# Performance work log

Measured on AMD Instinct MI355X. Metric: run time of the kernel, lower is better.

The kernel has to match this reference:

```python
import jax, jax.numpy as jnp
import numpy as np
from jax import lax

OBS_LEN = 20
N_COORD = 2
HIDDEN = 192  # z_dim + s_dim = 128 + 64
N = 131072


def setup_inputs() -> dict:
    key = jax.random.key(0)
    ks = jax.random.split(key, 6)
    obs_traj_rel = jax.random.normal(ks[0], (OBS_LEN, N, N_COORD), dtype=jnp.float32)
    pred_lstm_hidden = jax.random.normal(ks[1], (N, HIDDEN), dtype=jnp.float32)
    # LSTMCell params (torch layout: weight_ih [4H, in], weight_hh [4H, H])
    w_ih = jax.random.normal(ks[2], (4 * HIDDEN, N_COORD), dtype=jnp.float32) * 0.1
    w_hh = jax.random.normal(ks[3], (4 * HIDDEN, HIDDEN), dtype=jnp.float32) * 0.1
    b_ih = jnp.zeros((4 * HIDDEN,), dtype=jnp.float32)
    b_hh = jnp.zeros((4 * HIDDEN,), dtype=jnp.float32)
    # hidden2pos Linear
    w_out = jax.random.normal(ks[4], (N_COORD, HIDDEN), dtype=jnp.float32) * 0.1
    b_out = jnp.zeros((N_COORD,), dtype=jnp.float32)
    return {
        "obs_traj_rel": obs_traj_rel,
        "pred_lstm_hidden": pred_lstm_hidden,
        "w_ih": w_ih,
        "w_hh": w_hh,
        "b_ih": b_ih,
        "b_hh": b_hh,
        "w_out": w_out,
        "b_out": b_out,
    }


def reference(obs_traj_rel, pred_lstm_hidden, w_ih, w_hh, b_ih, b_hh, w_out, b_out):
    T = obs_traj_rel.shape[0]
    # step i uses obs_traj_rel[max(i-1, 0)] -> indices [0, 0, 1, ..., T-2]
    idx = jnp.concatenate([jnp.zeros((1,), jnp.int32), jnp.arange(T - 1, dtype=jnp.int32)])
    xs = obs_traj_rel[idx, :, :N_COORD]  # [T, N, 2]

    def step(carry, x_t):
        h, c = carry
        gates = x_t @ w_ih.T + b_ih + h @ w_hh.T + b_hh  # [N, 4H]
        i, f, g, o = jnp.split(gates, 4, axis=-1)  # torch LSTMCell gate order
        i = jax.nn.sigmoid(i)
        f = jax.nn.sigmoid(f)
        g = jnp.tanh(g)
        o = jax.nn.sigmoid(o)
        c_new = f * c + i * g
        h_new = o * jnp.tanh(c_new)
        out = h_new @ w_out.T + b_out  # [N, 2]
        return (h_new, c_new), out

    c0 = jnp.zeros_like(pred_lstm_hidden)
    (_, _), outs = lax.scan(step, (pred_lstm_hidden, c0), xs)
    return outs  # [T, N, 2]
```

## Files before the change

### kernel.cpp

```cpp
#include <hip/hip_runtime.h>

typedef _Float16 half8 __attribute__((ext_vector_type(8)));
typedef float floatx4 __attribute__((ext_vector_type(4)));

#define T_STEPS 20
#define NSEQ 131072
#define HID 192
#define ROWS 32
#define HPAD 200
#define HROWS 17
#define WOFF 147456
#define XOFF 150528
#define FR_TOTAL (XOFF + 6144)

#define MFMA16(a, b, c) __builtin_amdgcn_mfma_f32_16x16x32_f16((a), (b), (c), 0, 0, 0)

__global__ void build_frags(const float* __restrict__ whh,
                            const float* __restrict__ wout,
                            const float* __restrict__ wih,
                            const float* __restrict__ bih,
                            const float* __restrict__ bhh,
                            _Float16* __restrict__ dst) {
    int i = blockIdx.x * 256 + threadIdx.x;
    if (i < WOFF) {
        int e = i & 7, L = (i >> 3) & 63, g = (i >> 9) & 3, u = i >> 11;
        int kc = u % 6, ht = u / 6;
        int n = L & 15, q = L >> 4;
        dst[i] = (_Float16)whh[(size_t)(g * HID + ht * 16 + n) * HID + kc * 32 + q * 8 + e];
    } else if (i < XOFF) {
        int k = i - WOFF;
        int e = k & 7, L = (k >> 3) & 63, kc = k >> 9;
        int n = L & 15, q = L >> 4;
        dst[i] = (_Float16)((n < 2) ? wout[n * HID + kc * 32 + q * 8 + e] : 0.f);
    } else if (i < FR_TOTAL) {
        int k = i - XOFF;
        int e = k & 7, n = (k >> 3) & 15, g = (k >> 7) & 3, ht = k >> 9;
        int col = g * HID + ht * 16 + n;
        float v = 0.f;
        if (e == 0)      v = wih[col * 2];
        else if (e == 1) v = wih[col * 2 + 1];
        else if (e == 2) v = bih[col] + bhh[col];
        dst[i] = (_Float16)v;
    }
}

__global__ __launch_bounds__(768) __attribute__((amdgpu_waves_per_eu(3, 3)))
void lstm_fused_kernel(
    const float* __restrict__ obs,
    const float* __restrict__ h0,
    const float* __restrict__ b_out,
    const _Float16* __restrict__ frags,
    float* __restrict__ out)
{
    __shared__ _Float16 h0b[2][HROWS][HPAD];
    __shared__ _Float16 h1b[HROWS][HPAD];
    __shared__ _Float16 b_lds[49152];
    __shared__ _Float16 wo_lds[3072];
    __shared__ float2 x_all[T_STEPS][ROWS];

    const int tid  = threadIdx.x;
    const int wave = tid >> 6;
    const int lane = tid & 63;
    const int quad = lane >> 4;
    const int l16  = lane & 15;
    const int ht   = wave;
    const int base = blockIdx.x * ROWS;
    const int j    = ht * 16 + l16;

    const half8 HZ = {0, 0, 0, 0, 0, 0, 0, 0};

    half8 bw[16], bx[4];
#pragma unroll
    for (int kc = 0; kc < 4; ++kc)
#pragma unroll
        for (int g = 0; g < 4; ++g)
            bw[kc * 4 + g] = *(const half8*)&frags[(((ht * 6 + kc) * 4 + g) << 9) + lane * 8];
#pragma unroll
    for (int g = 0; g < 4; ++g)
        bx[g] = (quad == 0)
              ? *(const half8*)&frags[XOFF + ht * 512 + g * 128 + l16 * 8]
              : HZ;

    for (int i = tid; i < 2 * HROWS * HPAD / 8; i += 768) ((half8*)h0b)[i] = HZ;
    for (int i = tid; i < HROWS * HPAD / 8; i += 768)     ((half8*)h1b)[i] = HZ;
    for (int i = tid; i < 6144; i += 768) {
        int g = (i >> 6) & 3, u = i >> 8, k2 = u & 1, h = u >> 1;
        ((half8*)b_lds)[i] = *(const half8*)&frags[(((h * 6 + 4 + k2) * 4 + g) << 9) + (i & 63) * 8];
    }
    if (tid < 384) ((half8*)wo_lds)[tid] = *(const half8*)&frags[WOFF + tid * 8];
    if (tid < T_STEPS * ROWS) {
        int t = tid >> 5, r = tid & 31;
        int src = (t == 0) ? 0 : (t - 1);
        x_all[t][r] = *(const float2*)&obs[((size_t)src * NSEQ + base + r) * 2];
    }
    __syncthreads();

    for (int i = tid; i < ROWS * HID / 4; i += 768) {
        float4 v = *(const float4*)&h0[(size_t)base * HID + i * 4];
        int row = (i * 4) / HID, k = i * 4 - row * HID;
        _Float16* d = (row < 16) ? &h0b[0][row][k] : &h1b[row - 16][k];
        d[0] = (_Float16)v.x; d[1] = (_Float16)v.y;
        d[2] = (_Float16)v.z; d[3] = (_Float16)v.w;
    }
    if (tid < 64) {
        int row = tid >> 1;
        _Float16 v = (_Float16)((const float*)x_all[0])[tid];
        if (row < 16) h0b[0][row][192 + (tid & 1)] = v;
        else          h1b[row - 16][192 + (tid & 1)] = v;
    }
    if (tid < 16)      { h0b[0][tid][194] = (_Float16)1.f; h0b[1][tid][194] = (_Float16)1.f; }
    else if (tid < 32)   h1b[tid - 16][194] = (_Float16)1.f;
    __syncthreads();

    const float bo_n = (l16 < 2) ? b_out[l16] : 0.f;

    float c[8];
#pragma unroll
    for (int i = 0; i < 8; ++i) c[i] = 0.f;

    auto build = [&](const _Float16* hb, floatx4* aN) {
        const _Float16* ar = hb + l16 * HPAD;
        const _Float16* blp = b_lds;
        asm volatile("" : "+v"(blp));
#pragma unroll
        for (int g = 0; g < 4; ++g) aN[g] = (floatx4){0.f, 0.f, 0.f, 0.f};
        half8 ax = *(const half8*)(ar + 192 + quad * 8);
#pragma unroll
        for (int g = 0; g < 4; ++g)
            aN[g] = MFMA16(ax, bx[g], aN[g]);
#pragma unroll
        for (int kc = 0; kc < 4; ++kc) {
            half8 a = *(const half8*)(ar + kc * 32 + quad * 8);
#pragma unroll
            for (int g = 0; g < 4; ++g)
                aN[g] = MFMA16(a, bw[kc * 4 + g], aN[g]);
        }
#pragma unroll
        for (int k2 = 0; k2 < 2; ++k2) {
            half8 a = *(const half8*)(ar + (4 + k2) * 32 + quad * 8);
#pragma unroll
            for (int g = 0; g < 4; ++g) {
                half8 b = *(const half8*)&blp[(((ht * 2 + k2) * 4 + g) << 9) + lane * 8];
                aN[g] = MFMA16(a, b, aN[g]);
            }
        }
    };

    auto act = [&](floatx4* aO, _Float16* hw, int cb) {
#pragma unroll
        for (int r = 0; r < 4; ++r) {
            const int row = quad * 4 + r;
            const float Ai = __builtin_amdgcn_exp2f(-1.4426950408889634f * aO[0][r]);
            const float Af = __builtin_amdgcn_exp2f(-1.4426950408889634f * aO[1][r]);
            const float Bg = __builtin_amdgcn_exp2f( 2.8853900817779268f * aO[2][r]);
            const float Co = __builtin_amdgcn_exp2f(-1.4426950408889634f * aO[3][r]);
            const float Qf = 1.f + Af;
            const float Pg = (1.f + Ai) * (Bg + 1.f);
            const float Nn = c[cb + r] * Pg + Qf * (Bg - 1.f);
            const float cn = Nn * __builtin_amdgcn_rcpf(Qf * Pg);
            c[cb + r] = cn;
            const float Dc = __builtin_amdgcn_exp2f(2.8853900817779268f * cn);
            const float hv = (Dc - 1.f) * __builtin_amdgcn_rcpf((1.f + Co) * (Dc + 1.f));
            hw[row * HPAD + j] = (_Float16)hv;
        }
    };

    auto sched_pattern = [&]() {
#pragma unroll
        for (int u = 0; u < 7; ++u) {
            __builtin_amdgcn_sched_group_barrier(0x100, 2, 0);
            __builtin_amdgcn_sched_group_barrier(0x008, 4, 0);
            __builtin_amdgcn_sched_group_barrier(0x002, 16, 0);
        }
        __builtin_amdgcn_sched_group_barrier(0x200, 4, 0);
    };

    auto wout1 = [&](int ot, const _Float16* hbase) {
        const _Float16* ar = hbase + l16 * HPAD;
        floatx4 ao = {bo_n, bo_n, bo_n, bo_n};
#pragma unroll
        for (int kc = 0; kc < 6; ++kc) {
            half8 a = *(const half8*)(ar + kc * 32 + quad * 8);
            half8 b = *(const half8*)&wo_lds[kc * 512 + lane * 8];
            ao = MFMA16(a, b, ao);
        }
        if (l16 < 2) {
#pragma unroll
            for (int r = 0; r < 4; ++r)
                out[((size_t)ot * NSEQ + base + ht * 16 + quad * 4 + r) * 2 + l16] = ao[r];
        }
    };

    floatx4 accA[4], accB[4];
    build(&h0b[0][0][0], accA);

    for (int t = 0; t < T_STEPS - 1; ++t) {
        _Float16* h0n = &h0b[(t + 1) & 1][0][0];

        build(&h1b[0][0], accB);
        act(accA, h0n, 0);
        sched_pattern();
        if (ht < 2 && t > 0)
            wout1(t - 1, (ht == 0) ? &h0b[t & 1][0][0] : &h1b[0][0]);
        if (ht == 11 && lane < 32)
            h0n[(lane >> 1) * HPAD + 192 + (lane & 1)] =
                (_Float16)((const float*)x_all[t + 1])[lane];
        __syncthreads();

        build(h0n, accA);
        act(accB, &h1b[0][0], 4);
        sched_pattern();
        if (ht == 11 && lane < 32)
            h1b[lane >> 1][192 + (lane & 1)] =
                (_Float16)((const float*)x_all[t + 1])[32 + lane];
        __syncthreads();
    }

    build(&h1b[0][0], accB);
    act(accA, &h0b[0][0][0], 0);
    sched_pattern();
    if (ht < 2)
        wout1(18, (ht == 0) ? &h0b[1][0][0] : &h1b[0][0]);
    __syncthreads();
    act(accB, &h1b[0][0], 4);
    __syncthreads();
    if (ht < 2)
        wout1(19, (ht == 0) ? &h0b[0][0][0] : &h1b[0][0]);
}

extern "C" void kernel_launch(void* const* d_in, const int* in_sizes, int n_in,
                              void* d_out, int out_size, void* d_ws, size_t ws_size,
                              hipStream_t stream) {
    const float* obs  = (const float*)d_in[0];
    const float* h0   = (const float*)d_in[1];
    const float* wih  = (const float*)d_in[2];
    const float* whh  = (const float*)d_in[3];
    const float* bih  = (const float*)d_in[4];
    const float* bhh  = (const float*)d_in[5];
    const float* wout = (const float*)d_in[6];
    const float* bout = (const float*)d_in[7];
    float* out = (float*)d_out;
    _Float16* frags = (_Float16*)d_ws;

    build_frags<<<(FR_TOTAL + 255) / 256, 256, 0, stream>>>(whh, wout, wih, bih, bhh, frags);
    lstm_fused_kernel<<<NSEQ / ROWS, 768, 0, stream>>>(obs, h0, bout, frags, out);
}
```

Measured before the change: 1.190 ms.

## Keep all W_hh fragments in registers and fold input projection into FP32 init

All six K-chunks of the recurrent weight fragments now stay in registers, so the 96 KB LDS staging of the last two chunks and their per-step LDS reads go away. The input projection and bias, previously an extra MFMA over padded x/one columns, are now computed in FP32 with FMAs as the accumulator's starting value. The per-step writes of x into the h buffers and the padding row are removed, and the scheduling groups are adjusted to match. The cost is higher VGPR pressure from 24 resident half8 fragments, which may cause spills under the fixed waves-per-EU setting.

New measurement: 1.456 ms. 22.4% more time.

```diff
diff --git a/kernel.cpp b/kernel.cpp
--- a/kernel.cpp
+++ b/kernel.cpp
@@ -8,7 +8,6 @@
 #define HID 192
 #define ROWS 32
 #define HPAD 200
-#define HROWS 17
 #define WOFF 147456
 #define XOFF 150528
 #define FR_TOTAL (XOFF + 6144)
@@ -32,15 +31,6 @@
         int e = k & 7, L = (k >> 3) & 63, kc = k >> 9;
         int n = L & 15, q = L >> 4;
         dst[i] = (_Float16)((n < 2) ? wout[n * HID + kc * 32 + q * 8 + e] : 0.f);
-    } else if (i < FR_TOTAL) {
-        int k = i - XOFF;
-        int e = k & 7, n = (k >> 3) & 15, g = (k >> 7) & 3, ht = k >> 9;
-        int col = g * HID + ht * 16 + n;
-        float v = 0.f;
-        if (e == 0)      v = wih[col * 2];
-        else if (e == 1) v = wih[col * 2 + 1];
-        else if (e == 2) v = bih[col] + bhh[col];
-        dst[i] = (_Float16)v;
     }
 }
 
@@ -48,15 +38,17 @@
 void lstm_fused_kernel(
     const float* __restrict__ obs,
     const float* __restrict__ h0,
+    const float* __restrict__ w_ih,
+    const float* __restrict__ b_ih,
+    const float* __restrict__ b_hh,
     const float* __restrict__ b_out,
     const _Float16* __restrict__ frags,
     float* __restrict__ out)
 {
-    __shared__ _Float16 h0b[2][HROWS][HPAD];
-    __shared__ _Float16 h1b[HROWS][HPAD];
-    __shared__ _Float16 b_lds[49152];
+    __shared__ _Float16 h0b[2][16][HPAD];
+    __shared__ _Float16 h1b[16][HPAD];
     __shared__ _Float16 wo_lds[3072];
-    __shared__ float2 x_all[T_STEPS][ROWS];
+    __shared__ alignas(16) float2 x_all[T_STEPS][ROWS];
 
     const int tid  = threadIdx.x;
     const int wave = tid >> 6;
@@ -67,34 +59,28 @@
     const int base = blockIdx.x * ROWS;
     const int j    = ht * 16 + l16;
 
-    const half8 HZ = {0, 0, 0, 0, 0, 0, 0, 0};
-
-    half8 bw[16], bx[4];
-#pragma unroll
-    for (int kc = 0; kc < 4; ++kc)
+    half8 bw[24];
+#pragma unroll
+    for (int kc = 0; kc < 6; ++kc)
 #pragma unroll
         for (int g = 0; g < 4; ++g)
             bw[kc * 4 + g] = *(const half8*)&frags[(((ht * 6 + kc) * 4 + g) << 9) + lane * 8];
-#pragma unroll
-    for (int g = 0; g < 4; ++g)
-        bx[g] = (quad == 0)
-              ? *(const half8*)&frags[XOFF + ht * 512 + g * 128 + l16 * 8]
-              : HZ;
-
-    for (int i = tid; i < 2 * HROWS * HPAD / 8; i += 768) ((half8*)h0b)[i] = HZ;
-    for (int i = tid; i < HROWS * HPAD / 8; i += 768)     ((half8*)h1b)[i] = HZ;
-    for (int i = tid; i < 6144; i += 768) {
-        int g = (i >> 6) & 3, u = i >> 8, k2 = u & 1, h = u >> 1;
-        ((half8*)b_lds)[i] = *(const half8*)&frags[(((h * 6 + 4 + k2) * 4 + g) << 9) + (i & 63) * 8];
-    }
+
+    float bs[4], w0[4], w1[4];
+#pragma unroll
+    for (int g = 0; g < 4; ++g) {
+        bs[g] = b_ih[g * HID + j] + b_hh[g * HID + j];
+        w0[g] = w_ih[(g * HID + j) * 2];
+        w1[g] = w_ih[(g * HID + j) * 2 + 1];
+    }
+    const float bo_n = (l16 < 2) ? b_out[l16] : 0.f;
+
     if (tid < 384) ((half8*)wo_lds)[tid] = *(const half8*)&frags[WOFF + tid * 8];
     if (tid < T_STEPS * ROWS) {
         int t = tid >> 5, r = tid & 31;
         int src = (t == 0) ? 0 : (t - 1);
         x_all[t][r] = *(const float2*)&obs[((size_t)src * NSEQ + base + r) * 2];
     }
-    __syncthreads();
-
     for (int i = tid; i < ROWS * HID / 4; i += 768) {
         float4 v = *(const float4*)&h0[(size_t)base * HID + i * 4];
         int row = (i * 4) / HID, k = i * 4 - row * HID;
@@ -102,47 +88,29 @@
         d[0] = (_Float16)v.x; d[1] = (_Float16)v.y;
         d[2] = (_Float16)v.z; d[3] = (_Float16)v.w;
     }
-    if (tid < 64) {
-        int row = tid >> 1;
-        _Float16 v = (_Float16)((const float*)x_all[0])[tid];
-        if (row < 16) h0b[0][row][192 + (tid & 1)] = v;
-        else          h1b[row - 16][192 + (tid & 1)] = v;
-    }
-    if (tid < 16)      { h0b[0][tid][194] = (_Float16)1.f; h0b[1][tid][194] = (_Float16)1.f; }
-    else if (tid < 32)   h1b[tid - 16][194] = (_Float16)1.f;
     __syncthreads();
 
-    const float bo_n = (l16 < 2) ? b_out[l16] : 0.f;
-
     float c[8];
 #pragma unroll
     for (int i = 0; i < 8; ++i) c[i] = 0.f;
 
-    auto build = [&](const _Float16* hb, floatx4* aN) {
+    auto build = [&](const _Float16* hb, const float2* xr, floatx4* aN) {
         const _Float16* ar = hb + l16 * HPAD;
-        const _Float16* blp = b_lds;
-        asm volatile("" : "+v"(blp));
-#pragma unroll
-        for (int g = 0; g < 4; ++g) aN[g] = (floatx4){0.f, 0.f, 0.f, 0.f};
-        half8 ax = *(const half8*)(ar + 192 + quad * 8);
-#pragma unroll
-        for (int g = 0; g < 4; ++g)
-            aN[g] = MFMA16(ax, bx[g], aN[g]);
-#pragma unroll
-        for (int kc = 0; kc < 4; ++kc) {
+        float4 x01 = *(const float4*)&xr[quad * 4];
+        float4 x23 = *(const float4*)&xr[quad * 4 + 2];
+#pragma unroll
+        for (int g = 0; g < 4; ++g) {
+            aN[g][0] = bs[g] + x01.x * w0[g] + x01.y * w1[g];
+            aN[g][1] = bs[g] + x01.z * w0[g] + x01.w * w1[g];
+            aN[g][2] = bs[g] + x23.x * w0[g] + x23.y * w1[g];
+            aN[g][3] = bs[g] + x23.z * w0[g] + x23.w * w1[g];
+        }
+#pragma unroll
+        for (int kc = 0; kc < 6; ++kc) {
             half8 a = *(const half8*)(ar + kc * 32 + quad * 8);
 #pragma unroll
             for (int g = 0; g < 4; ++g)
                 aN[g] = MFMA16(a, bw[kc * 4 + g], aN[g]);
-        }
-#pragma unroll
-        for (int k2 = 0; k2 < 2; ++k2) {
-            half8 a = *(const half8*)(ar + (4 + k2) * 32 + quad * 8);
-#pragma unroll
-            for (int g = 0; g < 4; ++g) {
-                half8 b = *(const half8*)&blp[(((ht * 2 + k2) * 4 + g) << 9) + lane * 8];
-                aN[g] = MFMA16(a, b, aN[g]);
-            }
         }
     };
 
@@ -166,11 +134,12 @@
     };
 
     auto sched_pattern = [&]() {
-#pragma unroll
-        for (int u = 0; u < 7; ++u) {
-            __builtin_amdgcn_sched_group_barrier(0x100, 2, 0);
+        __builtin_amdgcn_sched_group_barrier(0x002, 12, 0);
+#pragma unroll
+        for (int u = 0; u < 6; ++u) {
+            __builtin_amdgcn_sched_group_barrier(0x100, 1, 0);
             __builtin_amdgcn_sched_group_barrier(0x008, 4, 0);
-            __builtin_amdgcn_sched_group_barrier(0x002, 16, 0);
+            __builtin_amdgcn_sched_group_barrier(0x002, 18, 0);
         }
         __builtin_amdgcn_sched_group_barrier(0x200, 4, 0);
     };
@@ -192,31 +161,25 @@
     };
 
     floatx4 accA[4], accB[4];
-    build(&h0b[0][0][0], accA);
+    build(&h0b[0][0][0], &x_all[0][0], accA);
 
     for (int t = 0; t < T_STEPS - 1; ++t) {
         _Float16* h0n = &h0b[(t + 1) & 1][0][0];
 
-        build(&h1b[0][0], accB);
+        build(&h1b[0][0], &x_all[t][16], accB);
         act(accA, h0n, 0);
         sched_pattern();
         if (ht < 2 && t > 0)
             wout1(t - 1, (ht == 0) ? &h0b[t & 1][0][0] : &h1b[0][0]);
-        if (ht == 11 && lane < 32)
-            h0n[(lane >> 1) * HPAD + 192 + (lane & 1)] =
-                (_Float16)((const float*)x_all[t + 1])[lane];
         __syncthreads();
 
-        build(h0n, accA);
+        build(h0n, &x_all[t + 1][0], accA);
         act(accB, &h1b[0][0], 4);
         sched_pattern();
-        if (ht == 11 && lane < 32)
-            h1b[lane >> 1][192 + (lane & 1)] =
-                (_Float16)((const float*)x_all[t + 1])[32 + lane];
         __syncthreads();
     }
 
-    build(&h1b[0][0], accB);
+    build(&h1b[0][0], &x_all[T_STEPS - 1][16], accB);
     act(accA, &h0b[0][0][0], 0);
     sched_pattern();
     if (ht < 2)
@@ -243,5 +206,6 @@
     _Float16* frags = (_Float16*)d_ws;
 
     build_frags<<<(FR_TOTAL + 255) / 256, 256, 0, stream>>>(whh, wout, wih, bih, bhh, frags);
-    lstm_fused_kernel<<<NSEQ / ROWS, 768, 0, stream>>>(obs, h0, bout, frags, out);
+    lstm_fused_kernel<<<NSEQ / ROWS, 768, 0, stream>>>(
+        obs, h0, wih, bih, bhh, bout, frags, out);
 }
```
